# Kernel tuning notes

Hardware: AMD Instinct MI355X
Metric: run time of the kernel (lower is better)

The kernel has to match this reference:

```python
import jax, jax.numpy as jnp
import numpy as np

B, T, K, DIM = 32, 12, 16, 512
H0, H1 = 512, 256


def setup_inputs() -> dict:
    key = jax.random.key(0)
    k0, k1, k2, k3, k4 = jax.random.split(key, 5)
    return {
        "sets_of_objects": jax.random.normal(k0, (B, T, K, DIM), dtype=jnp.float32),
        "W0": jax.random.normal(k1, (2 * DIM, H0), dtype=jnp.float32) * 0.02,
        "b0": jnp.zeros((H0,), dtype=jnp.float32),
        "W1": jax.random.normal(k2, (H0, H1), dtype=jnp.float32) * 0.02,
        "b1": jnp.zeros((H1,), dtype=jnp.float32),
        "D": DIM,
    }


def reference(sets_of_objects, W0, b0, W1, b1, D):
    Bb, Tt, Kk, Dm = sets_of_objects.shape
    Tm1 = Tt - 1
    # Eval path: for each t in 1..T-1, original code builds all-pairs concat of
    # O_t with itself (O_1 is unused in create_inter_object_cat), runs the MLP,
    # then avg-pools over t identical copies (no-op on e) and clamps the summed mask.
    O_t = sets_of_objects[:, 1:]                                   # [B, T-1, K, D]
    A = jnp.broadcast_to(O_t[:, :, :, None, :], (Bb, Tm1, Kk, Kk, Dm))   # first obj k repeated
    Bo = jnp.broadcast_to(O_t[:, :, None, :, :], (Bb, Tm1, Kk, Kk, Dm))  # second obj j
    pairs = jnp.concatenate([A, Bo], axis=-1).reshape(Bb, Tm1, Kk * Kk, 2 * Dm)
    # EncoderMLP: Linear -> ReLU per hidden layer
    h = jax.nn.relu(pairs @ W0 + b0)                               # [B, T-1, K*K, H0]
    e = jax.nn.relu(h @ W1 + b1)                                   # [B, T-1, K*K, H1]
    # object-presence masks (clamp of feature sums)
    is_first = jnp.clip(pairs[..., :D].sum(-1), 0.0, 1.0)          # [B, T-1, K*K]
    is_second = jnp.clip(pairs[..., D:].sum(-1), 0.0, 1.0)
    # clamp(sum over t identical copies, 0, 1) == clamp(t * v, 0, 1)
    counts = jnp.arange(1, Tt, dtype=e.dtype)[None, :, None]
    is_obj = jnp.clip(counts * is_first * is_second, 0.0, 1.0)
    return e, is_obj
```

## Files before the change

kernel.cpp:

```cpp
#include <hip/hip_runtime.h>
#include <hip/hip_bf16.h>

#define B_    32
#define T_    12
#define TM1   11
#define K_    16
#define DIM_  512
#define H0_   512
#define H1_   256
#define NROWS 5632
#define NBT   352
#define E_ELEMS (NBT*256*H1_)

typedef __bf16 bf16x8 __attribute__((ext_vector_type(8)));
typedef float  f32x16 __attribute__((ext_vector_type(16)));
typedef float  f32x4  __attribute__((ext_vector_type(4)));
typedef unsigned u32x4 __attribute__((ext_vector_type(4)));

#define OFRAG_OFF   0
#define W0FRAG_OFF  5767168
#define W1FRAG_OFF  (W0FRAG_OFF + 1048576)
#define UB_OFF      (W1FRAG_OFF + 262144)
#define VSW_OFF     (UB_OFF + 5767168)

__device__ __forceinline__ unsigned bf_rn(float f) {
    unsigned u = __float_as_uint(f);
    return (u + 0x7fffu + ((u >> 16) & 1u)) >> 16;
}
__device__ __forceinline__ unsigned pk_bf16(float lo, float hi) {
    return bf_rn(lo) | (bf_rn(hi) << 16);
}
__device__ __forceinline__ unsigned short f2bf(float f) {
    return (unsigned short)bf_rn(f);
}
__device__ __forceinline__ float bfu_lo(unsigned u) { return __uint_as_float(u << 16); }
__device__ __forceinline__ float bfu_hi(unsigned u) { return __uint_as_float(u & 0xffff0000u); }
__device__ __forceinline__ unsigned cvt_pk(float lo, float hi) {
    unsigned r;
    asm("v_cvt_pk_bf16_f32 %0, %1, %2" : "=v"(r) : "v"(lo), "v"(hi));
    return r;
}

__global__ __launch_bounds__(256) void k_prep(const float* __restrict__ W0,
                                              const float* __restrict__ W1,
                                              const float* __restrict__ O,
                                              char* __restrict__ ws)
{
    const int unit = blockIdx.x * 4 + (threadIdx.x >> 6);
    const int l = threadIdx.x & 63;
    if (unit < 1280) {
        const float* src; size_t dstoff; int stride;
        if (unit < 1024) {
            int half = unit >> 9, s = (unit >> 4) & 31, nt = unit & 15;
            int k = s*16 + (l >> 5)*8;
            int n = nt*32 + (l & 31);
            src = W0 + (size_t)(half*512 + k) * H0_ + n;
            stride = H0_;
            dstoff = W0FRAG_OFF + (((size_t)(half*32 + s)*16 + nt)*64 + l)*16;
        } else {
            int r = unit - 1024; int s = r >> 3, ct = r & 7;
            int k = s*16 + (l >> 5)*8;
            int n = ct*32 + (l & 31);
            src = W1 + (size_t)k * H1_ + n;
            stride = H1_;
            dstoff = W1FRAG_OFF + (((size_t)(s*8 + ct))*64 + l)*16;
        }
        float f[8];
        #pragma unroll
        for (int j = 0; j < 8; ++j) f[j] = src[(size_t)j * stride];
        u32x4 o = { pk_bf16(f[0],f[1]), pk_bf16(f[2],f[3]), pk_bf16(f[4],f[5]), pk_bf16(f[6],f[7]) };
        *(u32x4*)(ws + dstoff) = o;
    } else {
        const int u = unit - 1280;
        const int s = u / 176, mt = u % 176;
        const int row = mt*32 + (l & 31);
        const int b  = row / (TM1*K_);
        const int rem = row % (TM1*K_);
        const int t  = rem / K_;
        const int i  = rem % K_;
        const float* src = O + (((size_t)(b*T_ + t + 1)*K_ + i)*DIM_) + s*16 + (l >> 5)*8;
        float4 a = *(const float4*)src;
        float4 c = *(const float4*)(src + 4);
        u32x4 o = { pk_bf16(a.x,a.y), pk_bf16(a.z,a.w), pk_bf16(c.x,c.y), pk_bf16(c.z,c.w) };
        *(u32x4*)(ws + OFRAG_OFF + ((size_t)(s*176 + mt)*64 + l)*16) = o;
    }
}

__global__ __launch_bounds__(256) void k_uv(char* __restrict__ ws,
                                            const float* __restrict__ b0)
{
    const int mb = blockIdx.x;
    const int t  = threadIdx.x, l = t & 63;
    const int nb = blockIdx.y * 4 + (t >> 6);
    const int half = nb >> 3;
    const char* Ag = ws + OFRAG_OFF + ((size_t)(mb*2)*64 + l)*16;
    const char* Bg = ws + W0FRAG_OFF + (size_t)half*524288 + ((size_t)((nb&7)*2)*64 + l)*16;
    const size_t AS = 176*1024, BS = 16*1024;

    f32x16 acc[2][2];
    #pragma unroll
    for (int p = 0; p < 2; ++p)
        #pragma unroll
        for (int c = 0; c < 2; ++c)
            #pragma unroll
            for (int r = 0; r < 16; ++r) acc[p][c][r] = 0.f;

    u32x4 aA[2], bA[2], aB[2], bB[2];
    #pragma unroll
    for (int p = 0; p < 2; ++p) {
        aA[p] = *(const u32x4*)(Ag + 0*AS + p*1024);
        bA[p] = *(const u32x4*)(Bg + 0*BS + p*1024);
        aB[p] = *(const u32x4*)(Ag + 1*AS + p*1024);
        bB[p] = *(const u32x4*)(Bg + 1*BS + p*1024);
    }

    for (int ss = 0; ss < 32; ss += 2) {
        {
            union { u32x4 u[2]; bf16x8 b[2]; } af, bf;
            af.u[0]=aA[0]; af.u[1]=aA[1]; bf.u[0]=bA[0]; bf.u[1]=bA[1];
            if (ss + 2 < 32) {
                #pragma unroll
                for (int p = 0; p < 2; ++p) {
                    aA[p] = *(const u32x4*)(Ag + (size_t)(ss+2)*AS + p*1024);
                    bA[p] = *(const u32x4*)(Bg + (size_t)(ss+2)*BS + p*1024);
                }
            }
            acc[0][0] = __builtin_amdgcn_mfma_f32_32x32x16_bf16(af.b[0], bf.b[0], acc[0][0], 0,0,0);
            acc[0][1] = __builtin_amdgcn_mfma_f32_32x32x16_bf16(af.b[0], bf.b[1], acc[0][1], 0,0,0);
            acc[1][0] = __builtin_amdgcn_mfma_f32_32x32x16_bf16(af.b[1], bf.b[0], acc[1][0], 0,0,0);
            acc[1][1] = __builtin_amdgcn_mfma_f32_32x32x16_bf16(af.b[1], bf.b[1], acc[1][1], 0,0,0);
        }
        {
            union { u32x4 u[2]; bf16x8 b[2]; } af, bf;
            af.u[0]=aB[0]; af.u[1]=aB[1]; bf.u[0]=bB[0]; bf.u[1]=bB[1];
            if (ss + 3 < 32) {
                #pragma unroll
                for (int p = 0; p < 2; ++p) {
                    aB[p] = *(const u32x4*)(Ag + (size_t)(ss+3)*AS + p*1024);
                    bB[p] = *(const u32x4*)(Bg + (size_t)(ss+3)*BS + p*1024);
                }
            }
            acc[0][0] = __builtin_amdgcn_mfma_f32_32x32x16_bf16(af.b[0], bf.b[0], acc[0][0], 0,0,0);
            acc[0][1] = __builtin_amdgcn_mfma_f32_32x32x16_bf16(af.b[0], bf.b[1], acc[0][1], 0,0,0);
            acc[1][0] = __builtin_amdgcn_mfma_f32_32x32x16_bf16(af.b[1], bf.b[0], acc[1][0], 0,0,0);
            acc[1][1] = __builtin_amdgcn_mfma_f32_32x32x16_bf16(af.b[1], bf.b[1], acc[1][1], 0,0,0);
        }
    }

    #pragma unroll
    for (int p = 0; p < 2; ++p) {
        #pragma unroll
        for (int c = 0; c < 2; ++c) {
            const int col = (nb & 7)*64 + c*32 + (l & 31);
            const float bias = (half == 0) ? b0[col] : 0.f;
            #pragma unroll
            for (int r = 0; r < 16; ++r) {
                const int row = (r & 3) + 8*(r >> 2) + 4*(l >> 5);
                const int M = mb*64 + p*32 + row;
                const float v = acc[p][c][r] + bias;
                if (half == 0) {
                    *(unsigned short*)(ws + UB_OFF + ((size_t)M*512 + col)*2) = f2bf(v);
                } else {
                    const int bt = M >> 4, j = M & 15;
                    const int cc = col >> 3;
                    const int c2 = ((cc ^ (j & 7)) << 3) | (col & 7);
                    *(unsigned short*)(ws + VSW_OFF + ((size_t)(bt*16 + j)*512 + c2)*2) = f2bf(v);
                }
            }
        }
    }
}

__global__ __launch_bounds__(256) void k_obj(const float* __restrict__ O,
                                             float* __restrict__ out)
{
    __shared__ float red[16][16];
    __shared__ float fl[16];
    const int bt = blockIdx.x;
    const int b_ = bt / TM1, tt = bt % TM1;
    const int t  = threadIdx.x;
    const int i  = t >> 4, s = t & 15;
    const float* base = O + (((size_t)(b_ * T_ + tt + 1) * K_ + i) * DIM_) + s * 32;
    float sum = 0.f;
    #pragma unroll
    for (int q = 0; q < 8; ++q) {
        float4 v = *(const float4*)(base + q * 4);
        sum += v.x + v.y + v.z + v.w;
    }
    red[i][s] = sum;
    __syncthreads();
    if (t < 16) {
        float f = 0.f;
        #pragma unroll
        for (int s2 = 0; s2 < 16; ++s2) f += red[t][s2];
        fl[t] = fminf(fmaxf(f, 0.f), 1.f);
    }
    __syncthreads();
    const float val = fminf((float)(tt + 1) * fl[t >> 4] * fl[t & 15], 1.f);
    __builtin_nontemporal_store(val, out + (size_t)E_ELEMS + (size_t)bt * 256 + t);
}

#define KSTEP(S, WK)                                                           \
    do {                                                                       \
        const int vch_ = (((S)*2 + kc) ^ jlow_);                               \
        u32x4 vu_ = *(const u32x4*)(VsL + vch_*16);                            \
        u32x4 uu_ = *(const u32x4*)(UsL + (S)*32);                             \
        u32x4 o_;                                                              \
        _Pragma("unroll")                                                      \
        for (int q_ = 0; q_ < 4; ++q_) {                                       \
            float h0_ = fmaxf(bfu_lo(uu_[q_]) + bfu_lo(vu_[q_]), 0.f);         \
            float h1_ = fmaxf(bfu_hi(uu_[q_]) + bfu_hi(vu_[q_]), 0.f);         \
            o_[q_] = cvt_pk(h0_, h1_);                                         \
        }                                                                      \
        union { u32x4 u; bf16x8 b; } af_; af_.u = o_;                          \
        union { u32x4 u[4]; bf16x8 b[4]; } wu_;                                \
        _Pragma("unroll")                                                      \
        for (int c_ = 0; c_ < 4; ++c_) wu_.u[c_] = WK[c_];                     \
        acc0 = __builtin_amdgcn_mfma_f32_32x32x16_bf16(af_.b, wu_.b[0], acc0, 0,0,0); \
        acc1 = __builtin_amdgcn_mfma_f32_32x32x16_bf16(af_.b, wu_.b[1], acc1, 0,0,0); \
        acc2 = __builtin_amdgcn_mfma_f32_32x32x16_bf16(af_.b, wu_.b[2], acc2, 0,0,0); \
        acc3 = __builtin_amdgcn_mfma_f32_32x32x16_bf16(af_.b, wu_.b[3], acc3, 0,0,0); \
    } while (0)

__global__ __launch_bounds__(256, 3) void k_e(const char* __restrict__ ws,
                                              const float* __restrict__ b1,
                                              float* __restrict__ out)
{
    __shared__ alignas(16) char lds[24576];
    char* Us = lds;
    char* Vs = lds + 8192;

    const int bid = blockIdx.x;
    const int ch = bid & 1, ph = (bid >> 1) & 1, bt = bid >> 2;
    const int t = threadIdx.x, l = t & 63, wp = t >> 6;

    const char* Ug = ws + UB_OFF  + (size_t)(bt*16 + ph*8) * 1024;
    const char* Vg = ws + VSW_OFF + (size_t)bt * 16384;
    const char* Wg = ws + W1FRAG_OFF + (size_t)(ch*4)*1024 + (size_t)l*16;

    #pragma unroll
    for (int r = 0; r < 2; ++r) { int c = t + r*256; *(u32x4*)(Us + c*16) = *(const u32x4*)(Ug + c*16); }
    #pragma unroll
    for (int r = 0; r < 4; ++r) { int c = t + r*256; *(u32x4*)(Vs + c*16) = *(const u32x4*)(Vg + c*16); }
    __syncthreads();

    f32x16 acc0, acc1, acc2, acc3;
    #pragma unroll
    for (int r = 0; r < 16; ++r) { acc0[r] = 0.f; acc1[r] = 0.f; acc2[r] = 0.f; acc3[r] = 0.f; }

    const int jj   = l & 15;
    const int jlow_ = jj & 7;
    const int kc   = l >> 5;
    const int il   = wp*2 + ((l >> 4) & 1);
    const char* UsL = Us + il*1024 + kc*16;
    const char* VsL = Vs + jj*1024;

    u32x4 wA[4], wB[4];
    #pragma unroll
    for (int c = 0; c < 4; ++c) wA[c] = *(const u32x4*)(Wg + c*1024);

    for (int sj = 0; sj < 16; ++sj) {
        const int s0 = sj * 2;
        #pragma unroll
        for (int c = 0; c < 4; ++c)
            wB[c] = *(const u32x4*)(Wg + (size_t)(s0+1)*8192 + c*1024);
        KSTEP(s0, wA);
        if (sj < 15) {
            #pragma unroll
            for (int c = 0; c < 4; ++c)
                wA[c] = *(const u32x4*)(Wg + (size_t)(s0+2)*8192 + c*1024);
        }
        KSTEP(s0+1, wB);
    }

    const int colb = ch*128 + (l & 31);
    const int pr0  = ph*128 + wp*32 + 4*(l >> 5);
    float* ob = out + ((size_t)bt*256 + pr0)*256 + colb;
    #define EPI(ACC, CT)                                                       \
        do {                                                                   \
            const float bb_ = b1[colb + (CT)*32];                              \
            _Pragma("unroll")                                                  \
            for (int r_ = 0; r_ < 16; ++r_) {                                  \
                const int rr_ = (r_ & 3) + 8*(r_ >> 2);                        \
                __builtin_nontemporal_store(fmaxf(ACC[r_] + bb_, 0.f),         \
                    ob + (size_t)rr_*256 + (CT)*32);                           \
            }                                                                  \
        } while (0)
    EPI(acc0, 0);
    EPI(acc1, 1);
    EPI(acc2, 2);
    EPI(acc3, 3);
    #undef EPI
}

extern "C" void kernel_launch(void* const* d_in, const int* in_sizes, int n_in,
                              void* d_out, int out_size, void* d_ws, size_t ws_size,
                              hipStream_t stream) {
    const float* O  = (const float*)d_in[0];
    const float* W0 = (const float*)d_in[1];
    const float* b0 = (const float*)d_in[2];
    const float* W1 = (const float*)d_in[3];
    const float* b1 = (const float*)d_in[4];
    float* out = (float*)d_out;
    char* ws = (char*)d_ws;

    k_prep<<<1728, 256, 0, stream>>>(W0, W1, O, ws);
    dim3 guv(88, 4);
    k_uv<<<guv, 256, 0, stream>>>(ws, b0);
    k_obj<<<NBT, 256, 0, stream>>>(O, out);
    k_e<<<NBT * 4, 256, 0, stream>>>(ws, b1, out);
}
```

Measured before the change: 70.10 us.

## Stage W1 fragments cooperatively into double-buffered LDS via global_load_lds

In the second-layer kernel, each wave used to load the full W1 fragment stream straight from global memory into registers, so all four waves fetched the same weights. Now each wave loads one quarter of every chunk with asynchronous global-to-LDS loads into a two-slot LDS buffer, and all waves read the weights from LDS. Block barriers separate the buffer swaps. This cuts redundant global/L2 weight traffic and register pressure, at the cost of extra barriers, LDS reads and a larger LDS footprint (40 KB per block), which may limit occupancy.

```diff
diff --git a/kernel.cpp b/kernel.cpp
--- a/kernel.cpp
+++ b/kernel.cpp
@@ -39,6 +39,11 @@
     unsigned r;
     asm("v_cvt_pk_bf16_f32 %0, %1, %2" : "=v"(r) : "v"(lo), "v"(hi));
     return r;
+}
+__device__ __forceinline__ void gl2lds16(const char* g, char* l) {
+    __builtin_amdgcn_global_load_lds(
+        (const __attribute__((address_space(1))) unsigned*)(const void*)g,
+        (__attribute__((address_space(3))) unsigned*)(void*)l, 16, 0, 0);
 }
 
 __global__ __launch_bounds__(256) void k_prep(const float* __restrict__ W0,
@@ -200,7 +205,13 @@
     __builtin_nontemporal_store(val, out + (size_t)E_ELEMS + (size_t)bt * 256 + t);
 }
 
-#define KSTEP(S, WK)                                                           \
+#define WSTAGE(C, BUFOFF)                                                      \
+    do {                                                                       \
+        gl2lds16(Wsrc + (size_t)((C)*2 + 0)*8192, Wbuf + (BUFOFF) + wq*1024);  \
+        gl2lds16(Wsrc + (size_t)((C)*2 + 1)*8192, Wbuf + (BUFOFF) + 4096 + wq*1024); \
+    } while (0)
+
+#define KSTEP_L(S, BUFOFF, ST)                                                 \
     do {                                                                       \
         const int vch_ = (((S)*2 + kc) ^ jlow_);                               \
         u32x4 vu_ = *(const u32x4*)(VsL + vch_*16);                            \
@@ -215,7 +226,8 @@
         union { u32x4 u; bf16x8 b; } af_; af_.u = o_;                          \
         union { u32x4 u[4]; bf16x8 b[4]; } wu_;                                \
         _Pragma("unroll")                                                      \
-        for (int c_ = 0; c_ < 4; ++c_) wu_.u[c_] = WK[c_];                     \
+        for (int c_ = 0; c_ < 4; ++c_)                                         \
+            wu_.u[c_] = *(const u32x4*)(WlL + (BUFOFF) + (ST)*4096 + c_*1024); \
         acc0 = __builtin_amdgcn_mfma_f32_32x32x16_bf16(af_.b, wu_.b[0], acc0, 0,0,0); \
         acc1 = __builtin_amdgcn_mfma_f32_32x32x16_bf16(af_.b, wu_.b[1], acc1, 0,0,0); \
         acc2 = __builtin_amdgcn_mfma_f32_32x32x16_bf16(af_.b, wu_.b[2], acc2, 0,0,0); \
@@ -226,55 +238,53 @@
                                               const float* __restrict__ b1,
                                               float* __restrict__ out)
 {
-    __shared__ alignas(16) char lds[24576];
-    char* Us = lds;
-    char* Vs = lds + 8192;
+    __shared__ alignas(16) char lds[40960];
+    char* Us   = lds;
+    char* Vs   = lds + 8192;
+    char* Wbuf = lds + 24576;
 
     const int bid = blockIdx.x;
     const int ch = bid & 1, ph = (bid >> 1) & 1, bt = bid >> 2;
-    const int t = threadIdx.x, l = t & 63, wp = t >> 6;
+    const int t = threadIdx.x, l = t & 63, wq = t >> 6;
 
     const char* Ug = ws + UB_OFF  + (size_t)(bt*16 + ph*8) * 1024;
     const char* Vg = ws + VSW_OFF + (size_t)bt * 16384;
-    const char* Wg = ws + W1FRAG_OFF + (size_t)(ch*4)*1024 + (size_t)l*16;
+    const char* Wsrc = ws + W1FRAG_OFF + (size_t)ch*4096 + (size_t)wq*1024 + (size_t)l*16;
 
     #pragma unroll
     for (int r = 0; r < 2; ++r) { int c = t + r*256; *(u32x4*)(Us + c*16) = *(const u32x4*)(Ug + c*16); }
     #pragma unroll
     for (int r = 0; r < 4; ++r) { int c = t + r*256; *(u32x4*)(Vs + c*16) = *(const u32x4*)(Vg + c*16); }
+
+    WSTAGE(0, 0);
     __syncthreads();
 
     f32x16 acc0, acc1, acc2, acc3;
     #pragma unroll
     for (int r = 0; r < 16; ++r) { acc0[r] = 0.f; acc1[r] = 0.f; acc2[r] = 0.f; acc3[r] = 0.f; }
 
-    const int jj   = l & 15;
+    const int jj    = l & 15;
     const int jlow_ = jj & 7;
-    const int kc   = l >> 5;
-    const int il   = wp*2 + ((l >> 4) & 1);
+    const int kc    = l >> 5;
+    const int il    = wq*2 + ((l >> 4) & 1);
     const char* UsL = Us + il*1024 + kc*16;
     const char* VsL = Vs + jj*1024;
-
-    u32x4 wA[4], wB[4];
-    #pragma unroll
-    for (int c = 0; c < 4; ++c) wA[c] = *(const u32x4*)(Wg + c*1024);
-
-    for (int sj = 0; sj < 16; ++sj) {
-        const int s0 = sj * 2;
-        #pragma unroll
-        for (int c = 0; c < 4; ++c)
-            wB[c] = *(const u32x4*)(Wg + (size_t)(s0+1)*8192 + c*1024);
-        KSTEP(s0, wA);
-        if (sj < 15) {
-            #pragma unroll
-            for (int c = 0; c < 4; ++c)
-                wA[c] = *(const u32x4*)(Wg + (size_t)(s0+2)*8192 + c*1024);
-        }
-        KSTEP(s0+1, wB);
+    const char* WlL = Wbuf + (size_t)l*16;
+
+    for (int j = 0; j < 8; ++j) {
+        const int c0 = j*2;
+        if (c0 + 1 < 16) WSTAGE(c0+1, 8192);
+        KSTEP_L(c0*2+0, 0, 0);
+        KSTEP_L(c0*2+1, 0, 1);
+        __syncthreads();
+        if (c0 + 2 < 16) WSTAGE(c0+2, 0);
+        KSTEP_L(c0*2+2, 8192, 0);
+        KSTEP_L(c0*2+3, 8192, 1);
+        __syncthreads();
     }
 
     const int colb = ch*128 + (l & 31);
-    const int pr0  = ph*128 + wp*32 + 4*(l >> 5);
+    const int pr0  = ph*128 + wq*32 + 4*(l >> 5);
     float* ob = out + ((size_t)bt*256 + pr0)*256 + colb;
     #define EPI(ACC, CT)                                                       \
         do {                                                                   \
```

New measurement: 65.46 us. -6.6%, faster.
